# Kernel tuning notes

Measured on AMD Instinct MI355X. Metric: run time of the kernel, lower is better.

The kernel has to match this reference:

```python
import jax, jax.numpy as jnp
import numpy as np

N_NODES = 50000
N_EDGES = 800000
IN_CH, HID_CH, OUT_CH = 128, 128, 64


def setup_inputs() -> dict:
    key = jax.random.key(0)
    k1, k2, k3, k4, k5, k6 = jax.random.split(key, 6)
    x = jax.random.normal(k1, (N_NODES, IN_CH), dtype=jnp.float32)
    edge_index = jax.random.randint(k2, (2, N_EDGES), 0, N_NODES, dtype=jnp.int64)
    # Glorot init like PyG GCNConv; bias zeros-like but random small for test coverage
    s1 = jnp.sqrt(6.0 / (IN_CH + HID_CH)).astype(jnp.float32)
    s2 = jnp.sqrt(6.0 / (HID_CH + OUT_CH)).astype(jnp.float32)
    W1 = jax.random.uniform(k3, (IN_CH, HID_CH), jnp.float32, -s1, s1)
    b1 = jax.random.normal(k4, (HID_CH,), jnp.float32) * 0.01
    W2 = jax.random.uniform(k5, (HID_CH, OUT_CH), jnp.float32, -s2, s2)
    b2 = jax.random.normal(k6, (OUT_CH,), jnp.float32) * 0.01
    return {"x": x, "edge_index": edge_index, "W1": W1, "b1": b1, "W2": W2, "b2": b2}


def gcn_conv(x, edge_index, W, b):
    """PyG GCNConv: add self-loops, symmetric D^-1/2 (A+I) D^-1/2 normalization,
    then aggregate linearly-transformed neighbor features + bias."""
    n = x.shape[0]
    h = x @ W  # [N, F_out]
    src, dst = edge_index[0], edge_index[1]
    # degree counts self-loop (weight 1) plus in-edges at dst
    deg = 1.0 + jax.ops.segment_sum(jnp.ones_like(src, dtype=h.dtype), dst, num_segments=n)
    dinv = jax.lax.rsqrt(deg)  # deg >= 1, no zeros
    norm = dinv[src] * dinv[dst]  # [E]
    agg = jax.ops.segment_sum(h[src] * norm[:, None], dst, num_segments=n)
    # self-loop contribution: norm = dinv[i]*dinv[i] = 1/deg[i]
    return agg + h * (1.0 / deg)[:, None] + b


def reference(x, edge_index, W1, b1, W2, b2):
    # eval-mode forward: dropout is identity
    h = gcn_conv(x, edge_index, W1, b1)
    h = jax.nn.relu(h)
    out = gcn_conv(h, edge_index, W2, b2)
    return out
```

## Files before the change

kernel.cpp:

```cpp
#include <hip/hip_runtime.h>
#include <hip/hip_fp16.h>


typedef _Float16 f16;
typedef __attribute__((ext_vector_type(8))) _Float16 f16x8;
typedef __attribute__((ext_vector_type(4))) float f32x4;

__global__ __launch_bounds__(256) void deg_kernel(const int* __restrict__ dst,
                                                  int* __restrict__ deg, int E) {
    int e = blockIdx.x * 256 + threadIdx.x;
    if (e < E) atomicAdd(&deg[dst[e]], 1);
}

__global__ __launch_bounds__(1024) void scan1_kernel(const int* __restrict__ deg,
                                                     int* __restrict__ rowptr,
                                                     int* __restrict__ bsum,
                                                     float* __restrict__ dinv, int N) {
    __shared__ int wsum[16];
    const int tid = threadIdx.x, lane = tid & 63, wid = tid >> 6;
    const int idx = blockIdx.x * 1024 + tid;
    int v = (idx < N) ? deg[idx] : 0;
    if (idx < N) dinv[idx] = rsqrtf((float)v + 1.0f);
    int incl = v;
#pragma unroll
    for (int off = 1; off < 64; off <<= 1) {
        int t = __shfl_up(incl, off, 64);
        if (lane >= off) incl += t;
    }
    if (lane == 63) wsum[wid] = incl;
    __syncthreads();
    if (wid == 0) {
        int s = (lane < 16) ? wsum[lane] : 0;
#pragma unroll
        for (int off = 1; off < 16; off <<= 1) {
            int t = __shfl_up(s, off, 64);
            if (lane >= off) s += t;
        }
        if (lane < 16) wsum[lane] = s;
    }
    __syncthreads();
    int waveoff = (wid == 0) ? 0 : wsum[wid - 1];
    if (idx < N) rowptr[idx] = waveoff + incl - v;
    if (tid == 1023) bsum[blockIdx.x] = waveoff + incl;
}

__global__ __launch_bounds__(64) void scan2_kernel(int* __restrict__ bsum, int nb) {
    int lane = threadIdx.x;
    int v = (lane < nb) ? bsum[lane] : 0;
    int incl = v;
#pragma unroll
    for (int off = 1; off < 64; off <<= 1) {
        int t = __shfl_up(incl, off, 64);
        if (lane >= off) incl += t;
    }
    if (lane < nb) bsum[lane] = incl;
}

__global__ __launch_bounds__(1024) void scan3_kernel(int* __restrict__ rowptr,
                                                     const int* __restrict__ bsum,
                                                     int N, int nb) {
    int idx = blockIdx.x * 1024 + threadIdx.x;
    if (blockIdx.x > 0 && idx < N) rowptr[idx] += bsum[blockIdx.x - 1];
    if (idx == 0) rowptr[N] = bsum[nb - 1];
}

__global__ __launch_bounds__(256) void fill_kernel(const int* __restrict__ src,
                                                   const int* __restrict__ dst,
                                                   const float* __restrict__ dinv,
                                                   const int* __restrict__ rowptr,
                                                   int* __restrict__ cnt,
                                                   float2* __restrict__ pairs, int E) {
    int e = blockIdx.x * 256 + threadIdx.x;
    if (e >= E) return;
    int s = src[e], d = dst[e];
    int pos = rowptr[d] + atomicAdd(&cnt[d], 1);
    float2 p;
    p.x = __int_as_float(s);
    p.y = dinv[s] * dinv[d];
    pairs[pos] = p;
}

__global__ __launch_bounds__(256) void prep_w(const float* __restrict__ W1,
                                              const float* __restrict__ W2,
                                              f16* __restrict__ Wt1, f16* __restrict__ Wt2) {
    int i = blockIdx.x * 256 + threadIdx.x;
    if (i < 128 * 128) {
        int k = i >> 7, c = i & 127;
        Wt1[c * 136 + k] = (f16)W1[i];
    } else if (i < 128 * 128 + 128 * 64) {
        int j = i - 128 * 128;
        int k = j >> 6, c = j & 63;
        Wt2[c * 136 + k] = (f16)W2[j];
    }
}

template <int KOUT, bool F32IN>
__global__ __launch_bounds__(256) void gemm_kernel(const void* __restrict__ Xv,
                                                   const f16* __restrict__ Wt,
                                                   f16* __restrict__ H, int N) {
    constexpr int CT = KOUT / 16;
    __shared__ f16 Wl[KOUT * 136];
    const int tid = threadIdx.x;
    constexpr int CHUNKS = KOUT * 136 / 8;
    {
        const uint4* s = (const uint4*)Wt;
        uint4* d = (uint4*)Wl;
        for (int i = tid; i < CHUNKS; i += 256) d[i] = s[i];
    }
    __syncthreads();

    const int lane = tid & 63, wid = tid >> 6;
    const int c = lane & 15, kseg = lane >> 4;
    const int row0 = blockIdx.x * 64 + wid * 16;
    int arow = row0 + c;
    if (arow >= N) arow = N - 1;

    f32x4 acc[CT];
#pragma unroll
    for (int t = 0; t < CT; ++t) acc[t] = (f32x4){0.f, 0.f, 0.f, 0.f};

#pragma unroll
    for (int kt = 0; kt < 4; ++kt) {
        const int k0 = kt * 32;
        f16x8 a;
        if (F32IN) {
            const float* xp = (const float*)Xv + (long)arow * 128 + k0 + kseg * 8;
            float4 x0 = *(const float4*)xp;
            float4 x1 = *(const float4*)(xp + 4);
            a[0] = (f16)x0.x; a[1] = (f16)x0.y; a[2] = (f16)x0.z; a[3] = (f16)x0.w;
            a[4] = (f16)x1.x; a[5] = (f16)x1.y; a[6] = (f16)x1.z; a[7] = (f16)x1.w;
        } else {
            a = *(const f16x8*)((const f16*)Xv + (long)arow * 128 + k0 + kseg * 8);
        }
#pragma unroll
        for (int ct = 0; ct < CT; ++ct) {
            f16x8 b = *(const f16x8*)&Wl[(ct * 16 + c) * 136 + k0 + kseg * 8];
            acc[ct] = __builtin_amdgcn_mfma_f32_16x16x32_f16(a, b, acc[ct], 0, 0, 0);
        }
    }

    const int rbase = row0 + kseg * 4;
#pragma unroll
    for (int ct = 0; ct < CT; ++ct)
#pragma unroll
        for (int r = 0; r < 4; ++r) {
            int row = rbase + r;
            if (row < N) H[(long)row * KOUT + ct * 16 + c] = (f16)acc[ct][r];
        }
}

template <int F, bool RELU, bool OUTF16>
__global__ __launch_bounds__(256) void gather_kernel(const void* __restrict__ Hv,
                                                     const int* __restrict__ rowptr,
                                                     const float2* __restrict__ pairs,
                                                     const float* __restrict__ dinv,
                                                     const float* __restrict__ bias,
                                                     void* __restrict__ outv, int N) {
    const int wid = threadIdx.x >> 6;
    const int lane = threadIdx.x & 63;
    const int node = blockIdx.x * 4 + wid;
    if (node >= N) return;
    const int start = rowptr[node], end = rowptr[node + 1];

    if (F == 128) {
        const __half2* Hu = (const __half2*)Hv;
        float ax = 0.f, ay = 0.f;
        int e = start;
        for (; e + 3 < end; e += 4) {
            float2 p0 = pairs[e], p1 = pairs[e + 1], p2 = pairs[e + 2], p3 = pairs[e + 3];
            __half2 u0 = Hu[(long)__float_as_int(p0.x) * 64 + lane];
            __half2 u1 = Hu[(long)__float_as_int(p1.x) * 64 + lane];
            __half2 u2 = Hu[(long)__float_as_int(p2.x) * 64 + lane];
            __half2 u3 = Hu[(long)__float_as_int(p3.x) * 64 + lane];
            float2 f0 = __half22float2(u0), f1 = __half22float2(u1);
            float2 f2 = __half22float2(u2), f3 = __half22float2(u3);
            ax += f0.x * p0.y + f1.x * p1.y + f2.x * p2.y + f3.x * p3.y;
            ay += f0.y * p0.y + f1.y * p1.y + f2.y * p2.y + f3.y * p3.y;
        }
        for (; e < end; ++e) {
            float2 p0 = pairs[e];
            float2 f0 = __half22float2(Hu[(long)__float_as_int(p0.x) * 64 + lane]);
            ax += f0.x * p0.y;
            ay += f0.y * p0.y;
        }
        float di = dinv[node];
        float d2 = di * di;
        float2 fs = __half22float2(Hu[(long)node * 64 + lane]);
        float2 bz = ((const float2*)bias)[lane];
        float zx = ax + fs.x * d2 + bz.x;
        float zy = ay + fs.y * d2 + bz.y;
        if (RELU) { zx = fmaxf(zx, 0.f); zy = fmaxf(zy, 0.f); }
        if (OUTF16) {
            ((__half2*)outv)[(long)node * 64 + lane] = __float22half2_rn(make_float2(zx, zy));
        } else {
            float2 o = {zx, zy};
            ((float2*)outv)[(long)node * 64 + lane] = o;
        }
    } else {
        const __half* Hh = (const __half*)Hv;
        float acc = 0.f;
        int e = start;
        for (; e + 3 < end; e += 4) {
            float2 p0 = pairs[e], p1 = pairs[e + 1], p2 = pairs[e + 2], p3 = pairs[e + 3];
            float h0 = __half2float(Hh[(long)__float_as_int(p0.x) * 64 + lane]);
            float h1 = __half2float(Hh[(long)__float_as_int(p1.x) * 64 + lane]);
            float h2 = __half2float(Hh[(long)__float_as_int(p2.x) * 64 + lane]);
            float h3 = __half2float(Hh[(long)__float_as_int(p3.x) * 64 + lane]);
            acc += h0 * p0.y + h1 * p1.y + h2 * p2.y + h3 * p3.y;
        }
        for (; e < end; ++e) {
            float2 p0 = pairs[e];
            acc += __half2float(Hh[(long)__float_as_int(p0.x) * 64 + lane]) * p0.y;
        }
        float di = dinv[node];
        float z = acc + __half2float(Hh[(long)node * 64 + lane]) * (di * di) + bias[lane];
        if (RELU) z = fmaxf(z, 0.f);
        ((float*)outv)[(long)node * 64 + lane] = z;
    }
}

extern "C" void kernel_launch(void* const* d_in, const int* in_sizes, int n_in,
                              void* d_out, int out_size, void* d_ws, size_t ws_size,
                              hipStream_t stream) {
    const float* x  = (const float*)d_in[0];
    const int*   ei = (const int*)d_in[1];
    const float* W1 = (const float*)d_in[2];
    const float* b1 = (const float*)d_in[3];
    const float* W2 = (const float*)d_in[4];
    const float* b2 = (const float*)d_in[5];
    float* out = (float*)d_out;

    const int N = in_sizes[0] / 128;
    const int E = in_sizes[1] / 2;
    const int* src = ei;
    const int* dst = ei + E;
    const int NB = (N + 1023) / 1024;

    float* ws = (float*)d_ws;
    float2* pairs = (float2*)ws;
    long off = 2L * E;
    int* deg    = (int*)(ws + off); off += N;
    int* cnt    = (int*)(ws + off); off += N;
    int* rowptr = (int*)(ws + off); off += N + 1;
    int* bsum   = (int*)(ws + off); off += 64;
    float* dinv = ws + off;        off += N;
    off = (off + 3) & ~3L;
    f16* Wt1 = (f16*)(ws + off); off += (128 * 136) / 2;
    f16* Wt2 = (f16*)(ws + off); off += (64 * 136) / 2;
    f16* h1  = (f16*)(ws + off); off += (long)N * 64;
    f16* z1  = (f16*)(ws + off); off += (long)N * 64;
    f16* h2  = (f16*)(ws + off); off += (long)N * 32;

    hipMemsetAsync(deg, 0, 2L * N * sizeof(int), stream);
    prep_w<<<(128 * 128 + 128 * 64 + 255) / 256, 256, 0, stream>>>(W1, W2, Wt1, Wt2);
    deg_kernel<<<(E + 255) / 256, 256, 0, stream>>>(dst, deg, E);
    scan1_kernel<<<NB, 1024, 0, stream>>>(deg, rowptr, bsum, dinv, N);
    scan2_kernel<<<1, 64, 0, stream>>>(bsum, NB);
    scan3_kernel<<<NB, 1024, 0, stream>>>(rowptr, bsum, N, NB);
    fill_kernel<<<(E + 255) / 256, 256, 0, stream>>>(src, dst, dinv, rowptr, cnt, pairs, E);

    gemm_kernel<128, true><<<(N + 63) / 64, 256, 0, stream>>>(x, Wt1, h1, N);
    gather_kernel<128, true, true><<<(N + 3) / 4, 256, 0, stream>>>(h1, rowptr, pairs, dinv, b1, z1, N);

    gemm_kernel<64, false><<<(N + 63) / 64, 256, 0, stream>>>(z1, Wt2, h2, N);
    gather_kernel<64, false, false><<<(N + 3) / 4, 256, 0, stream>>>(h2, rowptr, pairs, dinv, b2, out, N);
}
```

Before: 262.5 us.

## Record in-row positions during degree count, merge scan passes, deepen gather unroll

The degree-count kernel now saves each edge's atomic return value as its slot within the destination row and also converts the weights, replacing the separate weight-prep kernel. This removes the second atomic pass over a count array in the CSR fill. The two small scan-fixup kernels are merged into one that reduces block sums per block. The gather loops are unrolled to 8 edges so more loads are in flight. These changes cut kernel launches and atomics but add an E-sized position buffer and some extra register pressure in the gather.

```diff
diff --git a/kernel.cpp b/kernel.cpp
--- a/kernel.cpp
+++ b/kernel.cpp
@@ -6,10 +6,23 @@
 typedef __attribute__((ext_vector_type(8))) _Float16 f16x8;
 typedef __attribute__((ext_vector_type(4))) float f32x4;
 
-__global__ __launch_bounds__(256) void deg_kernel(const int* __restrict__ dst,
-                                                  int* __restrict__ deg, int E) {
-    int e = blockIdx.x * 256 + threadIdx.x;
-    if (e < E) atomicAdd(&deg[dst[e]], 1);
+__global__ __launch_bounds__(256) void deg_prep_kernel(const int* __restrict__ dst,
+                                                       int* __restrict__ deg,
+                                                       int* __restrict__ posw,
+                                                       const float* __restrict__ W1,
+                                                       const float* __restrict__ W2,
+                                                       f16* __restrict__ Wt1,
+                                                       f16* __restrict__ Wt2, int E) {
+    int gid = blockIdx.x * 256 + threadIdx.x;
+    if (gid < E) posw[gid] = atomicAdd(&deg[dst[gid]], 1);
+    if (gid < 128 * 128) {
+        int k = gid >> 7, c = gid & 127;
+        Wt1[c * 136 + k] = (f16)W1[gid];
+    } else if (gid < 128 * 128 + 128 * 64) {
+        int j = gid - 128 * 128;
+        int k = j >> 6, c = j & 63;
+        Wt2[c * 136 + k] = (f16)W2[j];
+    }
 }
 
 __global__ __launch_bounds__(1024) void scan1_kernel(const int* __restrict__ deg,
@@ -44,54 +57,42 @@
     if (tid == 1023) bsum[blockIdx.x] = waveoff + incl;
 }
 
-__global__ __launch_bounds__(64) void scan2_kernel(int* __restrict__ bsum, int nb) {
-    int lane = threadIdx.x;
-    int v = (lane < nb) ? bsum[lane] : 0;
-    int incl = v;
-#pragma unroll
-    for (int off = 1; off < 64; off <<= 1) {
-        int t = __shfl_up(incl, off, 64);
-        if (lane >= off) incl += t;
-    }
-    if (lane < nb) bsum[lane] = incl;
-}
-
-__global__ __launch_bounds__(1024) void scan3_kernel(int* __restrict__ rowptr,
-                                                     const int* __restrict__ bsum,
-                                                     int N, int nb) {
-    int idx = blockIdx.x * 1024 + threadIdx.x;
-    if (blockIdx.x > 0 && idx < N) rowptr[idx] += bsum[blockIdx.x - 1];
-    if (idx == 0) rowptr[N] = bsum[nb - 1];
+__global__ __launch_bounds__(1024) void scan23_kernel(int* __restrict__ rowptr,
+                                                      const int* __restrict__ bsum,
+                                                      int N, int nb) {
+    __shared__ int pfx_s;
+    const int tid = threadIdx.x;
+    if (tid < 64) {
+        int v = (tid < nb && tid < blockIdx.x) ? bsum[tid] : 0;
+#pragma unroll
+        for (int off = 32; off; off >>= 1) v += __shfl_xor(v, off, 64);
+        if (tid == 0) pfx_s = v;
+    }
+    if (blockIdx.x == 0 && tid >= 64 && tid < 128) {
+        int l = tid - 64;
+        int v = (l < nb) ? bsum[l] : 0;
+#pragma unroll
+        for (int off = 32; off; off >>= 1) v += __shfl_xor(v, off, 64);
+        if (l == 0) rowptr[N] = v;
+    }
+    __syncthreads();
+    int idx = blockIdx.x * 1024 + tid;
+    if (idx < N) rowptr[idx] += pfx_s;
 }
 
 __global__ __launch_bounds__(256) void fill_kernel(const int* __restrict__ src,
                                                    const int* __restrict__ dst,
+                                                   const int* __restrict__ posw,
                                                    const float* __restrict__ dinv,
                                                    const int* __restrict__ rowptr,
-                                                   int* __restrict__ cnt,
                                                    float2* __restrict__ pairs, int E) {
     int e = blockIdx.x * 256 + threadIdx.x;
     if (e >= E) return;
     int s = src[e], d = dst[e];
-    int pos = rowptr[d] + atomicAdd(&cnt[d], 1);
     float2 p;
     p.x = __int_as_float(s);
     p.y = dinv[s] * dinv[d];
-    pairs[pos] = p;
-}
-
-__global__ __launch_bounds__(256) void prep_w(const float* __restrict__ W1,
-                                              const float* __restrict__ W2,
-                                              f16* __restrict__ Wt1, f16* __restrict__ Wt2) {
-    int i = blockIdx.x * 256 + threadIdx.x;
-    if (i < 128 * 128) {
-        int k = i >> 7, c = i & 127;
-        Wt1[c * 136 + k] = (f16)W1[i];
-    } else if (i < 128 * 128 + 128 * 64) {
-        int j = i - 128 * 128;
-        int k = j >> 6, c = j & 63;
-        Wt2[c * 136 + k] = (f16)W2[j];
-    }
+    pairs[rowptr[d] + posw[e]] = p;
 }
 
 template <int KOUT, bool F32IN>
@@ -166,16 +167,33 @@
         const __half2* Hu = (const __half2*)Hv;
         float ax = 0.f, ay = 0.f;
         int e = start;
+        for (; e + 7 < end; e += 8) {
+            float2 pp[8];
+            __half2 uu[8];
+#pragma unroll
+            for (int j = 0; j < 8; ++j) pp[j] = pairs[e + j];
+#pragma unroll
+            for (int j = 0; j < 8; ++j) uu[j] = Hu[(long)__float_as_int(pp[j].x) * 64 + lane];
+#pragma unroll
+            for (int j = 0; j < 8; ++j) {
+                float2 f = __half22float2(uu[j]);
+                ax += f.x * pp[j].y;
+                ay += f.y * pp[j].y;
+            }
+        }
         for (; e + 3 < end; e += 4) {
-            float2 p0 = pairs[e], p1 = pairs[e + 1], p2 = pairs[e + 2], p3 = pairs[e + 3];
-            __half2 u0 = Hu[(long)__float_as_int(p0.x) * 64 + lane];
-            __half2 u1 = Hu[(long)__float_as_int(p1.x) * 64 + lane];
-            __half2 u2 = Hu[(long)__float_as_int(p2.x) * 64 + lane];
-            __half2 u3 = Hu[(long)__float_as_int(p3.x) * 64 + lane];
-            float2 f0 = __half22float2(u0), f1 = __half22float2(u1);
-            float2 f2 = __half22float2(u2), f3 = __half22float2(u3);
-            ax += f0.x * p0.y + f1.x * p1.y + f2.x * p2.y + f3.x * p3.y;
-            ay += f0.y * p0.y + f1.y * p1.y + f2.y * p2.y + f3.y * p3.y;
+            float2 pp[4];
+            __half2 uu[4];
+#pragma unroll
+            for (int j = 0; j < 4; ++j) pp[j] = pairs[e + j];
+#pragma unroll
+            for (int j = 0; j < 4; ++j) uu[j] = Hu[(long)__float_as_int(pp[j].x) * 64 + lane];
+#pragma unroll
+            for (int j = 0; j < 4; ++j) {
+                float2 f = __half22float2(uu[j]);
+                ax += f.x * pp[j].y;
+                ay += f.y * pp[j].y;
+            }
         }
         for (; e < end; ++e) {
             float2 p0 = pairs[e];
@@ -200,13 +218,25 @@
         const __half* Hh = (const __half*)Hv;
         float acc = 0.f;
         int e = start;
+        for (; e + 7 < end; e += 8) {
+            float2 pp[8];
+            __half uu[8];
+#pragma unroll
+            for (int j = 0; j < 8; ++j) pp[j] = pairs[e + j];
+#pragma unroll
+            for (int j = 0; j < 8; ++j) uu[j] = Hh[(long)__float_as_int(pp[j].x) * 64 + lane];
+#pragma unroll
+            for (int j = 0; j < 8; ++j) acc += __half2float(uu[j]) * pp[j].y;
+        }
         for (; e + 3 < end; e += 4) {
-            float2 p0 = pairs[e], p1 = pairs[e + 1], p2 = pairs[e + 2], p3 = pairs[e + 3];
-            float h0 = __half2float(Hh[(long)__float_as_int(p0.x) * 64 + lane]);
-            float h1 = __half2float(Hh[(long)__float_as_int(p1.x) * 64 + lane]);
-            float h2 = __half2float(Hh[(long)__float_as_int(p2.x) * 64 + lane]);
-            float h3 = __half2float(Hh[(long)__float_as_int(p3.x) * 64 + lane]);
-            acc += h0 * p0.y + h1 * p1.y + h2 * p2.y + h3 * p3.y;
+            float2 pp[4];
+            __half uu[4];
+#pragma unroll
+            for (int j = 0; j < 4; ++j) pp[j] = pairs[e + j];
+#pragma unroll
+            for (int j = 0; j < 4; ++j) uu[j] = Hh[(long)__float_as_int(pp[j].x) * 64 + lane];
+#pragma unroll
+            for (int j = 0; j < 4; ++j) acc += __half2float(uu[j]) * pp[j].y;
         }
         for (; e < end; ++e) {
             float2 p0 = pairs[e];
@@ -239,8 +269,8 @@
     float* ws = (float*)d_ws;
     float2* pairs = (float2*)ws;
     long off = 2L * E;
+    int* posw   = (int*)(ws + off); off += E;
     int* deg    = (int*)(ws + off); off += N;
-    int* cnt    = (int*)(ws + off); off += N;
     int* rowptr = (int*)(ws + off); off += N + 1;
     int* bsum   = (int*)(ws + off); off += 64;
     float* dinv = ws + off;        off += N;
@@ -251,13 +281,11 @@
     f16* z1  = (f16*)(ws + off); off += (long)N * 64;
     f16* h2  = (f16*)(ws + off); off += (long)N * 32;
 
-    hipMemsetAsync(deg, 0, 2L * N * sizeof(int), stream);
-    prep_w<<<(128 * 128 + 128 * 64 + 255) / 256, 256, 0, stream>>>(W1, W2, Wt1, Wt2);
-    deg_kernel<<<(E + 255) / 256, 256, 0, stream>>>(dst, deg, E);
+    hipMemsetAsync(deg, 0, (size_t)N * sizeof(int), stream);
+    deg_prep_kernel<<<(E + 255) / 256, 256, 0, stream>>>(dst, deg, posw, W1, W2, Wt1, Wt2, E);
     scan1_kernel<<<NB, 1024, 0, stream>>>(deg, rowptr, bsum, dinv, N);
-    scan2_kernel<<<1, 64, 0, stream>>>(bsum, NB);
-    scan3_kernel<<<NB, 1024, 0, stream>>>(rowptr, bsum, N, NB);
-    fill_kernel<<<(E + 255) / 256, 256, 0, stream>>>(src, dst, dinv, rowptr, cnt, pairs, E);
+    scan23_kernel<<<NB, 1024, 0, stream>>>(rowptr, bsum, N, NB);
+    fill_kernel<<<(E + 255) / 256, 256, 0, stream>>>(src, dst, posw, dinv, rowptr, pairs, E);
 
     gemm_kernel<128, true><<<(N + 63) / 64, 256, 0, stream>>>(x, Wt1, h1, N);
     gather_kernel<128, true, true><<<(N + 3) / 4, 256, 0, stream>>>(h1, rowptr, pairs, dinv, b1, z1, N);
```

Measured after the change: 228.2 us. 1.15x faster.
